# Performance work log

Measured on AMD Instinct MI355X. Metric: run time of the kernel, lower is better.

## Reference

```python
import jax, jax.numpy as jnp
import numpy as np

N = 100000   # nodes
E = 1600000  # edges
D_IN = 256
H = 64       # hidden_dim


def _segment_softmax(e, dst, n):
    # e: [E, heads]; softmax over edges sharing the same dst node
    m = jax.ops.segment_max(e, dst, num_segments=n)
    m = jnp.where(jnp.isfinite(m), m, jnp.zeros_like(m))
    ex = jnp.exp(e - m[dst])
    s = jax.ops.segment_sum(ex, dst, num_segments=n)
    return ex / (s[dst] + 1e-16)


def gat_conv(x, edge_index, W, att_src, att_dst, bias, heads, odim):
    # PyG GATConv, concat=False (mean over heads), with self-loops, neg_slope=0.2
    n = x.shape[0]
    loop = jnp.arange(n, dtype=edge_index.dtype)
    src = jnp.concatenate([edge_index[0], loop])
    dst = jnp.concatenate([edge_index[1], loop])
    h = (x @ W).reshape(n, heads, odim)                      # [N, heads, odim]
    a_s = jnp.einsum('nhd,hd->nh', h, att_src)               # [N, heads]
    a_d = jnp.einsum('nhd,hd->nh', h, att_dst)
    e = jax.nn.leaky_relu(a_s[src] + a_d[dst], 0.2)          # [E+N, heads]
    alpha = _segment_softmax(e, dst, n)
    msg = h[src] * alpha[:, :, None]                         # gather + weight
    out = jax.ops.segment_sum(msg, dst, num_segments=n)      # scatter-reduce
    return out.mean(axis=1) + bias                           # concat=False -> mean


def gcn_conv(x, edge_index, W, bias):
    # PyG GCNConv with self-loops and symmetric normalization
    n = x.shape[0]
    loop = jnp.arange(n, dtype=edge_index.dtype)
    src = jnp.concatenate([edge_index[0], loop])
    dst = jnp.concatenate([edge_index[1], loop])
    deg = jax.ops.segment_sum(jnp.ones(src.shape[0], x.dtype), dst, num_segments=n)
    dinv = jnp.where(deg > 0, deg ** -0.5, jnp.zeros_like(deg))
    norm = dinv[src] * dinv[dst]                             # [E+N]
    h = x @ W
    return jax.ops.segment_sum(h[src] * norm[:, None], dst, num_segments=n) + bias


def setup_inputs() -> dict:
    key = jax.random.key(0)
    ks = jax.random.split(key, 16)
    f = lambda k, shp, s=0.05: (jax.random.normal(k, shp, dtype=jnp.float32) * s)
    inp = {
        'x': jax.random.normal(ks[0], (N, D_IN), dtype=jnp.float32),
        'edge_index': jax.random.randint(ks[1], (2, E), 0, N, dtype=jnp.int64),
        # GAT layer 1: heads=4, out=H
        'W1': f(ks[2], (D_IN, 4 * H)), 'a1s': f(ks[3], (4, H)), 'a1d': f(ks[4], (4, H)),
        'b1': jnp.zeros((H,), jnp.float32),
        # GAT layer 2: heads=2, out=H
        'W2': f(ks[5], (H, 2 * H)), 'a2s': f(ks[6], (2, H)), 'a2d': f(ks[7], (2, H)),
        'b2': jnp.zeros((H,), jnp.float32),
        # GCN layer: H -> H//2
        'Wg': f(ks[8], (H, H // 2)), 'bg': jnp.zeros((H // 2,), jnp.float32),
        # MLP head: H//2 -> H//4 -> 1
        'Wh1': f(ks[9], (H // 2, H // 4)), 'bh1': jnp.zeros((H // 4,), jnp.float32),
        'Wh2': f(ks[10], (H // 4, 1)), 'bh2': jnp.zeros((1,), jnp.float32),
    }
    return inp


def reference(x, edge_index, W1, a1s, a1d, b1, W2, a2s, a2d, b2, Wg, bg, Wh1, bh1, Wh2, bh2):
    h1 = jax.nn.relu(gat_conv(x, edge_index, W1, a1s, a1d, b1, heads=4, odim=H))
    h2 = jax.nn.relu(gat_conv(h1, edge_index, W2, a2s, a2d, b2, heads=2, odim=H))
    h3 = jax.nn.relu(gcn_conv(h2, edge_index, Wg, bg))
    z = jax.nn.relu(h3 @ Wh1 + bh1)
    svi = jax.nn.sigmoid(z @ Wh2 + bh2)
    return svi.squeeze(-1)
```

## Files before the change

### kernel.cpp

```cpp
#include <hip/hip_runtime.h>
#include <math.h>

static inline int cdiv(int a, int b){ return (a + b - 1) / b; }

typedef __attribute__((ext_vector_type(8))) short short8_t;
typedef __attribute__((ext_vector_type(4))) float f32x4;
typedef __attribute__((ext_vector_type(2))) float f32x2;

static __device__ inline unsigned short f2bf(float f) {
    union { float f; unsigned u; } v; v.f = f;
    unsigned r = v.u + 0x7fff + ((v.u >> 16) & 1);
    return (unsigned short)(r >> 16);
}

static __device__ inline unsigned char f2fp8(float f) {
    union { float f; unsigned u; } v; v.f = f;
    unsigned s = (v.u >> 24) & 0x80u;
    v.u &= 0x7fffffffu;
    v.f = fminf(v.f, 448.f);
    unsigned out;
    if (v.u >= (121u << 23)) {
        unsigned u = v.u + 0x7FFFFu + ((v.u >> 20) & 1u);
        out = (((u >> 23) - 120u) << 3) | ((u >> 20) & 7u);
    } else {
        out = (unsigned)(v.f * 512.f + 0.5f);
    }
    return (unsigned char)(out | s);
}

static __device__ inline float fp8_1(unsigned b) {
    unsigned s = (b & 0x80u) << 24;
    unsigned em = b & 0x7fu;
    union { unsigned u; float f; } n;
    n.u = (((em >> 3) + 120u) << 23) | ((em & 7u) << 20);
    float mag = (em >= 8u) ? n.f : (float)em * 0.001953125f;
    union { unsigned u; float f; } r; r.f = mag; r.u |= s;
    return r.f;
}

static __device__ __forceinline__ f32x2 fp8lo(unsigned v) {
#if __has_builtin(__builtin_amdgcn_cvt_pk_f32_fp8)
    return __builtin_amdgcn_cvt_pk_f32_fp8((int)v, false);
#else
    f32x2 r; r[0] = fp8_1(v & 0xff); r[1] = fp8_1((v >> 8) & 0xff); return r;
#endif
}
static __device__ __forceinline__ f32x2 fp8hi(unsigned v) {
#if __has_builtin(__builtin_amdgcn_cvt_pk_f32_fp8)
    return __builtin_amdgcn_cvt_pk_f32_fp8((int)v, true);
#else
    f32x2 r; r[0] = fp8_1((v >> 16) & 0xff); r[1] = fp8_1(v >> 24); return r;
#endif
}


__global__ __launch_bounds__(256) void k_count_deg_win(const int* __restrict__ dst, int E,
        int* __restrict__ deg, int wsize) {
    int win   = blockIdx.x & 7;
    int chunk = blockIdx.x >> 3;
    int lo = win * wsize, hi = lo + wsize;
    int base = (chunk * 256 + threadIdx.x) * 4;
    if (base + 3 < E) {
        int4 d = *(const int4*)(dst + base);
        if (d.x >= lo && d.x < hi) atomicAdd(&deg[d.x], 1);
        if (d.y >= lo && d.y < hi) atomicAdd(&deg[d.y], 1);
        if (d.z >= lo && d.z < hi) atomicAdd(&deg[d.z], 1);
        if (d.w >= lo && d.w < hi) atomicAdd(&deg[d.w], 1);
    } else {
        for (int k = 0; k < 4; k++) {
            int e = base + k;
            if (e < E) { int d = dst[e]; if (d >= lo && d < hi) atomicAdd(&deg[d], 1); }
        }
    }
}

__global__ void k_scan_partial(const int* __restrict__ deg, int n, int* __restrict__ partial) {
    __shared__ int sd[256];
    int base = blockIdx.x * 1024;
    int sum = 0;
    for (int i = threadIdx.x; i < 1024; i += 256) {
        int idx = base + i;
        if (idx < n) sum += deg[idx] + 1;
    }
    sd[threadIdx.x] = sum;
    __syncthreads();
    for (int s = 128; s > 0; s >>= 1) {
        if (threadIdx.x < s) sd[threadIdx.x] += sd[threadIdx.x + s];
        __syncthreads();
    }
    if (threadIdx.x == 0) partial[blockIdx.x] = sd[0];
}

__global__ void k_scan_top(int* __restrict__ partial, int nb, int* __restrict__ offs, int n) {
    if (blockIdx.x == 0 && threadIdx.x == 0) {
        int run = 0;
        for (int i = 0; i < nb; i++) { int v = partial[i]; partial[i] = run; run += v; }
        offs[n] = run;
    }
}

__global__ void k_scan_final(const int* __restrict__ deg, int n,
                             const int* __restrict__ partial, int* __restrict__ offs,
                             int* __restrict__ cursor, int* __restrict__ csr,
                             float* __restrict__ dinv) {
    __shared__ int sd[256];
    int tid = threadIdx.x;
    int base = blockIdx.x * 1024;
    int v[4]; int s0 = 0;
    #pragma unroll
    for (int j = 0; j < 4; j++) {
        int idx = base + tid*4 + j;
        v[j] = (idx < n) ? (deg[idx] + 1) : 0;
        s0 += v[j];
    }
    sd[tid] = s0;
    __syncthreads();
    for (int st = 1; st < 256; st <<= 1) {
        int t = (tid >= st) ? sd[tid - st] : 0;
        __syncthreads();
        sd[tid] += t;
        __syncthreads();
    }
    int ex = (tid > 0 ? sd[tid - 1] : 0) + partial[blockIdx.x];
    #pragma unroll
    for (int j = 0; j < 4; j++) {
        int idx = base + tid*4 + j;
        if (idx < n) {
            offs[idx]   = ex;
            cursor[idx] = ex;
            dinv[idx]   = rsqrtf((float)v[j]);
            csr[ex + v[j] - 1] = idx;
        }
        ex += v[j];
    }
}

__global__ __launch_bounds__(256) void k_fill_csr_win(const int* __restrict__ src,
        const int* __restrict__ dst, int E,
        int* __restrict__ cursor, int* __restrict__ csr, int wsize) {
    int win   = blockIdx.x & 7;
    int chunk = blockIdx.x >> 3;
    int lo = win * wsize, hi = lo + wsize;
    int base = (chunk * 256 + threadIdx.x) * 4;
    if (base + 3 < E) {
        int4 d = *(const int4*)(dst + base);
        bool ix = d.x >= lo && d.x < hi, iy = d.y >= lo && d.y < hi;
        bool iz = d.z >= lo && d.z < hi, iw = d.w >= lo && d.w < hi;
        if (ix | iy | iz | iw) {
            int4 s = *(const int4*)(src + base);
            if (ix) { int p = atomicAdd(&cursor[d.x], 1); csr[p] = s.x; }
            if (iy) { int p = atomicAdd(&cursor[d.y], 1); csr[p] = s.y; }
            if (iz) { int p = atomicAdd(&cursor[d.z], 1); csr[p] = s.z; }
            if (iw) { int p = atomicAdd(&cursor[d.w], 1); csr[p] = s.w; }
        }
    } else {
        for (int k = 0; k < 4; k++) {
            int e = base + k;
            if (e < E) {
                int d = dst[e];
                if (d >= lo && d < hi) { int p = atomicAdd(&cursor[d], 1); csr[p] = src[e]; }
            }
        }
    }
}


__global__ void k_prep_all(const float* __restrict__ W1, const float* __restrict__ W2,
                           const float* __restrict__ Wg, unsigned short* __restrict__ W1t,
                           unsigned short* __restrict__ W2t, unsigned short* __restrict__ Wgt) {
    int t = blockIdx.x * 256 + threadIdx.x;
    if (t < 65536) {
        int k = t >> 8, c = t & 255;
        W1t[c * 256 + k] = f2bf(W1[t]);
    }
    if (t < 8192) {
        int k = t >> 7, c = t & 127;
        W2t[c * 64 + k] = f2bf(W2[t]);
    }
    if (t < 2048) {
        int k = t >> 5, c = t & 31;
        Wgt[c * 64 + k] = f2bf(Wg[t]);
    }
}

__global__ __launch_bounds__(512) void k_gemm1_mfma(const float* __restrict__ A,
        const unsigned short* __restrict__ Bt, const float* __restrict__ att_s_g,
        const float* __restrict__ att_d_g, unsigned char* __restrict__ C,
        float* __restrict__ out_as, float* __restrict__ out_ad, int M) {
    constexpr int LDP = 40;
    __shared__ __align__(16) unsigned short As[128 * LDP];
    __shared__ __align__(16) unsigned short Bs[256 * LDP];
    __shared__ float att_l[512];
    int tid = threadIdx.x;
    int bm = blockIdx.x * 128;
    int wave = tid >> 6, lane = tid & 63;
    int wr = wave >> 1, wc = wave & 1;
    int lg = lane >> 4, lr = lane & 15;

    att_l[tid] = (tid < 256) ? att_s_g[tid] : att_d_g[tid - 256];

    f32x4 acc[2][8] = {};

    for (int k0 = 0; k0 < 256; k0 += 32) {
        __syncthreads();
        {
            int row = tid >> 2, part = tid & 3;
            int gr = bm + row;
            float4 v0, v1;
            if (gr < M) {
                const float4* p = (const float4*)(A + (size_t)gr * 256 + k0 + part * 8);
                v0 = p[0]; v1 = p[1];
            } else {
                v0 = make_float4(0.f,0.f,0.f,0.f); v1 = v0;
            }
            unsigned short* w = &As[row * LDP + part * 8];
            w[0]=f2bf(v0.x); w[1]=f2bf(v0.y); w[2]=f2bf(v0.z); w[3]=f2bf(v0.w);
            w[4]=f2bf(v1.x); w[5]=f2bf(v1.y); w[6]=f2bf(v1.z); w[7]=f2bf(v1.w);
        }
        {
            int col = tid >> 1, part = tid & 1;
            const uint4* p = (const uint4*)(Bt + (size_t)col * 256 + k0 + part * 16);
            uint4 u0 = p[0], u1 = p[1];
            *(uint4*)&Bs[col * LDP + part * 16]     = u0;
            *(uint4*)&Bs[col * LDP + part * 16 + 8] = u1;
        }
        __syncthreads();
        short8_t a[2], b[8];
        #pragma unroll
        for (int i = 0; i < 2; i++)
            a[i] = *(const short8_t*)&As[(wr * 32 + i * 16 + lr) * LDP + lg * 8];
        #pragma unroll
        for (int j = 0; j < 8; j++)
            b[j] = *(const short8_t*)&Bs[(wc * 128 + j * 16 + lr) * LDP + lg * 8];
        #pragma unroll
        for (int i = 0; i < 2; i++)
            #pragma unroll
            for (int j = 0; j < 8; j++)
                acc[i][j] = __builtin_amdgcn_mfma_f32_16x16x32_bf16(a[i], b[j], acc[i][j], 0, 0, 0);
    }
    float ws[8], wd[8];
    #pragma unroll
    for (int j = 0; j < 8; j++) {
        int c = wc * 128 + j * 16 + lr;
        ws[j] = att_l[c]; wd[j] = att_l[256 + c];
    }
    #pragma unroll
    for (int i = 0; i < 2; i++) {
        #pragma unroll
        for (int b2 = 0; b2 < 4; b2++) {
            int row = bm + wr * 32 + i * 16 + lg * 4 + b2;
            #pragma unroll
            for (int j = 0; j < 8; j++) {
                int col = wc * 128 + j * 16 + lr;
                if (row < M) C[(size_t)row * 256 + col] = f2fp8(acc[i][j][b2]);
            }
            float s0=0.f, s1=0.f, d0=0.f, d1=0.f;
            #pragma unroll
            for (int j = 0; j < 4; j++) { float v = acc[i][j][b2];   s0 += v*ws[j];   d0 += v*wd[j]; }
            #pragma unroll
            for (int j = 4; j < 8; j++) { float v = acc[i][j][b2];   s1 += v*ws[j];   d1 += v*wd[j]; }
            #pragma unroll
            for (int off = 1; off < 16; off <<= 1) {
                s0 += __shfl_xor(s0, off); s1 += __shfl_xor(s1, off);
                d0 += __shfl_xor(d0, off); d1 += __shfl_xor(d1, off);
            }
            if (lr == 0 && row < M) {
                out_as[row * 4 + wc * 2]     = s0;
                out_as[row * 4 + wc * 2 + 1] = s1;
                out_ad[row * 4 + wc * 2]     = d0;
                out_ad[row * 4 + wc * 2 + 1] = d1;
            }
        }
    }
}


template<int NC, bool ATT>
__global__ __launch_bounds__(256) void k_gemm_k64_mfma(const float* __restrict__ A,
        const unsigned short* __restrict__ Bt,
        const float* __restrict__ att_s_g, const float* __restrict__ att_d_g,
        unsigned char* __restrict__ C, float* __restrict__ out_as,
        float* __restrict__ out_ad, int M) {
    constexpr int NF  = NC / 16;
    constexpr int LDP = 72;
    __shared__ __align__(16) unsigned short As[64 * LDP];
    __shared__ __align__(16) unsigned short Bs[NC * LDP];
    __shared__ float att_l[ATT ? 2 * NC : 1];
    int tid = threadIdx.x;
    int bm = blockIdx.x * 64;
    int wave = tid >> 6, lane = tid & 63, lg = lane >> 4, lr = lane & 15;

    if constexpr (ATT) {
        if (tid < 2 * NC)
            att_l[tid] = (tid < NC) ? att_s_g[tid] : att_d_g[tid - NC];
    }
    {
        int row = tid >> 2, part = tid & 3;
        int gr = bm + row;
        float4 v0, v1, v2, v3;
        if (gr < M) {
            const float4* p = (const float4*)(A + (size_t)gr * 64 + part * 16);
            v0 = p[0]; v1 = p[1]; v2 = p[2]; v3 = p[3];
        } else {
            v0 = make_float4(0.f,0.f,0.f,0.f); v1 = v0; v2 = v0; v3 = v0;
        }
        unsigned short* w = &As[row * LDP + part * 16];
        w[0]=f2bf(v0.x);  w[1]=f2bf(v0.y);  w[2]=f2bf(v0.z);  w[3]=f2bf(v0.w);
        w[4]=f2bf(v1.x);  w[5]=f2bf(v1.y);  w[6]=f2bf(v1.z);  w[7]=f2bf(v1.w);
        w[8]=f2bf(v2.x);  w[9]=f2bf(v2.y);  w[10]=f2bf(v2.z); w[11]=f2bf(v2.w);
        w[12]=f2bf(v3.x); w[13]=f2bf(v3.y); w[14]=f2bf(v3.z); w[15]=f2bf(v3.w);
    }
    for (int i = tid; i < NC * 8; i += 256) {
        int c = i >> 3, part = i & 7;
        *(uint4*)&Bs[c * LDP + part * 8] = *(const uint4*)(Bt + (size_t)c * 64 + part * 8);
    }
    __syncthreads();

    f32x4 acc[NF] = {};
    short8_t a0 = *(const short8_t*)&As[(wave * 16 + lr) * LDP + lg * 8];
    short8_t a1 = *(const short8_t*)&As[(wave * 16 + lr) * LDP + 32 + lg * 8];
    #pragma unroll
    for (int j = 0; j < NF; j++) {
        short8_t b0 = *(const short8_t*)&Bs[(j * 16 + lr) * LDP + lg * 8];
        short8_t b1 = *(const short8_t*)&Bs[(j * 16 + lr) * LDP + 32 + lg * 8];
        acc[j] = __builtin_amdgcn_mfma_f32_16x16x32_bf16(a0, b0, acc[j], 0, 0, 0);
        acc[j] = __builtin_amdgcn_mfma_f32_16x16x32_bf16(a1, b1, acc[j], 0, 0, 0);
    }
    float ws[NF], wd[NF];
    if constexpr (ATT) {
        #pragma unroll
        for (int j = 0; j < NF; j++) { ws[j] = att_l[j * 16 + lr]; wd[j] = att_l[NC + j * 16 + lr]; }
    }
    #pragma unroll
    for (int b2 = 0; b2 < 4; b2++) {
        int row = bm + wave * 16 + lg * 4 + b2;
        #pragma unroll
        for (int j = 0; j < NF; j++)
            if (row < M) C[(size_t)row * NC + j * 16 + lr] = f2fp8(acc[j][b2]);
        if constexpr (ATT) {
            float s0=0.f, s1=0.f, d0=0.f, d1=0.f;
            #pragma unroll
            for (int j = 0; j < 4; j++) { float v = acc[j][b2]; s0 += v*ws[j]; d0 += v*wd[j]; }
            #pragma unroll
            for (int j = 4; j < 8; j++) { float v = acc[j][b2]; s1 += v*ws[j]; d1 += v*wd[j]; }
            #pragma unroll
            for (int off = 1; off < 16; off <<= 1) {
                s0 += __shfl_xor(s0, off); s1 += __shfl_xor(s1, off);
                d0 += __shfl_xor(d0, off); d1 += __shfl_xor(d1, off);
            }
            if (lr == 0 && row < M) {
                out_as[row * 2]     = s0;
                out_as[row * 2 + 1] = s1;
                out_ad[row * 2]     = d0;
                out_ad[row * 2 + 1] = d1;
            }
        }
    }
}


template<int HEADS>
__global__ __launch_bounds__(256) void k_gat_fused(const unsigned char* __restrict__ hpre,
        const float* __restrict__ as_n, const float* __restrict__ ad_n,
        const float* __restrict__ bias,
        const int* __restrict__ offs, const int* __restrict__ csr,
        float* __restrict__ out, int n_nodes) {
    __shared__ int   s_off[4][64];
    __shared__ float s_p[4][64 * HEADS];
    int wif  = threadIdx.x >> 6;
    int lane = threadIdx.x & 63;
    int n = blockIdx.x * 4 + wif;
    if (n >= n_nodes) return;
    const int beg = offs[n];
    const int deg = offs[n + 1] - beg;

    int h_id, dq;
    if constexpr (HEADS == 4) { h_id = lane >> 4; dq = lane & 15; }
    else                      { h_id = lane >> 5; dq = lane & 31; }
    const int lane_off = h_id * 64 + dq * 4;

    float adv[HEADS];
    if constexpr (HEADS == 4) {
        float4 t = *(const float4*)(ad_n + (size_t)n * 4);
        adv[0]=t.x; adv[1]=t.y; adv[2]=t.z; adv[3]=t.w;
    } else {
        float2 t = *(const float2*)(ad_n + (size_t)n * 2);
        adv[0]=t.x; adv[1]=t.y;
    }

    float sumh = 0.f;
    float acc[HEADS] = {};

    for (int j0 = 0; j0 < deg; j0 += 64) {
        int j = j0 + lane;
        int cnt = min(64, deg - j0);
        if (j < deg) {
            int s = csr[beg + j];
            s_off[wif][lane] = s * (HEADS * 64);
            float ev[HEADS];
            if constexpr (HEADS == 4) {
                float4 t = *(const float4*)(as_n + (size_t)s * 4);
                ev[0]=t.x; ev[1]=t.y; ev[2]=t.z; ev[3]=t.w;
            } else {
                float2 t = *(const float2*)(as_n + (size_t)s * 2);
                ev[0]=t.x; ev[1]=t.y;
            }
            #pragma unroll
            for (int h = 0; h < HEADS; h++) {
                float e = ev[h] + adv[h];
                e = fmaxf(e, 0.2f * e);
                s_p[wif][lane * HEADS + h] = __expf(e);
            }
        }
        #pragma unroll 4
        for (int q = 0; q < cnt; q++) {
            int off = s_off[wif][q];
            float p = s_p[wif][q * HEADS + h_id];
            sumh += p;
            if constexpr (HEADS == 4) {
                unsigned v = *(const unsigned*)(hpre + off + lane_off);
                f32x2 l = fp8lo(v), h2 = fp8hi(v);
                acc[0] += p * l[0]; acc[1] += p * l[1];
                acc[2] += p * h2[0]; acc[3] += p * h2[1];
            } else {
                unsigned v = *(const unsigned short*)(hpre + off + (lane_off >> 1));
                f32x2 l = fp8lo(v);
                acc[0] += p * l[0]; acc[1] += p * l[1];
            }
        }
    }
    float inv = 1.0f / (sumh + 1e-16f);
    float r[HEADS];
    #pragma unroll
    for (int c = 0; c < HEADS; c++) r[c] = acc[c] * inv;
    if constexpr (HEADS == 4) {
        #pragma unroll
        for (int c = 0; c < 4; c++) {
            r[c] += __shfl_xor(r[c], 16);
            r[c] += __shfl_xor(r[c], 32);
            r[c] *= 0.25f;
        }
        if (h_id == 0) {
            float4 b = *(const float4*)(bias + dq * 4);
            float4 o;
            o.x = fmaxf(r[0] + b.x, 0.f); o.y = fmaxf(r[1] + b.y, 0.f);
            o.z = fmaxf(r[2] + b.z, 0.f); o.w = fmaxf(r[3] + b.w, 0.f);
            *(float4*)(out + (size_t)n * 64 + dq * 4) = o;
        }
    } else {
        #pragma unroll
        for (int c = 0; c < 2; c++) {
            r[c] += __shfl_xor(r[c], 32);
            r[c] *= 0.5f;
        }
        if (h_id == 0) {
            float2 b = *(const float2*)(bias + dq * 2);
            float2 o;
            o.x = fmaxf(r[0] + b.x, 0.f); o.y = fmaxf(r[1] + b.y, 0.f);
            *(float2*)(out + (size_t)n * 64 + dq * 2) = o;
        }
    }
}


__global__ __launch_bounds__(256) void k_gcn_agg(const unsigned char* __restrict__ hpre,
        const float* __restrict__ dinv, const float* __restrict__ bias,
        const int* __restrict__ offs, const int* __restrict__ csr,
        float* __restrict__ out, int n_nodes) {
    int gid = blockIdx.x * 256 + threadIdx.x;
    int n = gid >> 3, q = gid & 7;
    if (n >= n_nodes) return;
    const int beg = offs[n], end = offs[n + 1];
    float4 acc = make_float4(0.f,0.f,0.f,0.f);
    #pragma unroll 4
    for (int j = beg; j < end; j++) {
        int s = csr[j];
        float ds = dinv[s];
        unsigned v = *(const unsigned*)(hpre + (size_t)s * 32 + q * 4);
        f32x2 l = fp8lo(v), h2 = fp8hi(v);
        acc.x += ds * l[0]; acc.y += ds * l[1];
        acc.z += ds * h2[0]; acc.w += ds * h2[1];
    }
    float dn = dinv[n];
    float4 b = *(const float4*)(bias + q * 4);
    float4 o;
    o.x = fmaxf(acc.x * dn + b.x, 0.f); o.y = fmaxf(acc.y * dn + b.y, 0.f);
    o.z = fmaxf(acc.z * dn + b.z, 0.f); o.w = fmaxf(acc.w * dn + b.w, 0.f);
    *(float4*)(out + (size_t)n * 32 + q * 4) = o;
}


__global__ __launch_bounds__(256) void k_mlp(const float* __restrict__ h3,
        const float* __restrict__ Wh1, const float* __restrict__ bh1,
        const float* __restrict__ Wh2, const float* __restrict__ bh2,
        float* __restrict__ out, int n_nodes) {
    __shared__ float w1[512];
    __shared__ float w2[16];
    __shared__ float b1s[16];
    __shared__ float b2s;
    int tid = threadIdx.x;
    for (int i = tid; i < 512; i += 256) w1[i] = Wh1[i];
    if (tid < 16) { w2[tid] = Wh2[tid]; b1s[tid] = bh1[tid]; }
    if (tid == 0) b2s = bh2[0];
    __syncthreads();
    int n = blockIdx.x * 256 + tid;
    if (n >= n_nodes) return;
    float x[32];
    const float4* p = (const float4*)(h3 + (size_t)n * 32);
    #pragma unroll
    for (int q = 0; q < 8; q++) { float4 v = p[q]; x[4*q] = v.x; x[4*q+1] = v.y; x[4*q+2] = v.z; x[4*q+3] = v.w; }
    float acc2 = b2s;
    #pragma unroll
    for (int j = 0; j < 16; j++) {
        float z = b1s[j];
        #pragma unroll
        for (int k = 0; k < 32; k++) z += x[k] * w1[k * 16 + j];
        z = fmaxf(z, 0.f);
        acc2 += z * w2[j];
    }
    out[n] = 1.0f / (1.0f + expf(-acc2));
}


extern "C" void kernel_launch(void* const* d_in, const int* in_sizes, int n_in,
                              void* d_out, int out_size, void* d_ws, size_t ws_size,
                              hipStream_t stream) {
    const float* x   = (const float*)d_in[0];
    const int*   ei  = (const int*)d_in[1];
    const float* W1  = (const float*)d_in[2];
    const float* a1s = (const float*)d_in[3];
    const float* a1d = (const float*)d_in[4];
    const float* b1  = (const float*)d_in[5];
    const float* W2  = (const float*)d_in[6];
    const float* a2s = (const float*)d_in[7];
    const float* a2d = (const float*)d_in[8];
    const float* b2  = (const float*)d_in[9];
    const float* Wg  = (const float*)d_in[10];
    const float* bg  = (const float*)d_in[11];
    const float* Wh1 = (const float*)d_in[12];
    const float* bh1 = (const float*)d_in[13];
    const float* Wh2 = (const float*)d_in[14];
    const float* bh2 = (const float*)d_in[15];

    const int N = in_sizes[0] / 256;
    const int E = in_sizes[1] / 2;
    const int* srcs = ei;
    const int* dsts = ei + E;

    float* R0   = (float*)d_ws;
    float* R1   = R0 + (size_t)N * 256;
    float* R2   = R1 + (size_t)N * 64;
    float* As_  = R2 + (size_t)N * 64;
    float* Ad_  = As_ + (size_t)N * 4;
    float* dinv = Ad_ + (size_t)N * 4;
    int* deg    = (int*)(dinv + N);
    int* offs   = deg + N;
    int* cursor = offs + (N + 1);
    int* csr    = cursor + N;
    int* parts  = csr + (E + N);
    unsigned short* W1t = (unsigned short*)(parts + 256);
    unsigned short* W2t = W1t + 65536;
    unsigned short* Wgt = W2t + 8192;
    unsigned char*  HP  = (unsigned char*)R0;

    int wsize = cdiv(N, 8);
    hipMemsetAsync(deg, 0, (size_t)N * sizeof(int), stream);
    k_count_deg_win<<<cdiv(E, 1024) * 8, 256, 0, stream>>>(dsts, E, deg, wsize);
    int nch = cdiv(N, 1024);
    k_scan_partial<<<nch, 256, 0, stream>>>(deg, N, parts);
    k_scan_top<<<1, 64, 0, stream>>>(parts, nch, offs, N);
    k_scan_final<<<nch, 256, 0, stream>>>(deg, N, parts, offs, cursor, csr, dinv);
    k_fill_csr_win<<<cdiv(E, 1024) * 8, 256, 0, stream>>>(srcs, dsts, E, cursor, csr, wsize);

    k_prep_all<<<256, 256, 0, stream>>>(W1, W2, Wg, W1t, W2t, Wgt);

    k_gemm1_mfma<<<cdiv(N, 128), 512, 0, stream>>>(x, W1t, a1s, a1d, HP, As_, Ad_, N);
    k_gat_fused<4><<<cdiv(N, 4), 256, 0, stream>>>(HP, As_, Ad_, b1, offs, csr, R1, N);

    k_gemm_k64_mfma<128, true><<<cdiv(N, 64), 256, 0, stream>>>(R1, W2t, a2s, a2d, HP, As_, Ad_, N);
    k_gat_fused<2><<<cdiv(N, 4), 256, 0, stream>>>(HP, As_, Ad_, b2, offs, csr, R2, N);

    k_gemm_k64_mfma<32, false><<<cdiv(N, 64), 256, 0, stream>>>(R2, Wgt, nullptr, nullptr, HP, nullptr, nullptr, N);
    k_gcn_agg<<<cdiv(N * 8, 256), 256, 0, stream>>>(HP, dinv, bg, offs, csr, R1, N);

    k_mlp<<<cdiv(N, 256), 256, 0, stream>>>(R1, Wh1, bh1, Wh2, bh2, (float*)d_out, N);
}
```

Baseline: 404.7 us.

## Fuse prep/scan launches, pack two nodes per wave in GAT2, fuse GCN with MLP

Folds the weight-transpose prep into the degree-count kernel and removes the single-thread scan_top kernel by having each scan_final block reduce its prefix from the partials. Layer-2 GAT now processes two nodes per wave, so all 64 lanes do useful work with 4-byte fp8 loads instead of 2-byte ones. The GCN aggregation is fused with the MLP head using cross-lane shuffles, which removes a kernel launch and the h3 round trip through memory. The costs are redundant prefix summation in every scan block and more shuffle work in the fused GCN kernel.

```diff
diff --git a/kernel.cpp b/kernel.cpp
--- a/kernel.cpp
+++ b/kernel.cpp
@@ -54,8 +54,18 @@
 }
 
 
-__global__ __launch_bounds__(256) void k_count_deg_win(const int* __restrict__ dst, int E,
-        int* __restrict__ deg, int wsize) {
+__global__ __launch_bounds__(256) void k_count_prep(const int* __restrict__ dst, int E,
+        int* __restrict__ deg, int wsize, int fillBlocks,
+        const float* __restrict__ W1, const float* __restrict__ W2,
+        const float* __restrict__ Wg, unsigned short* __restrict__ W1t,
+        unsigned short* __restrict__ W2t, unsigned short* __restrict__ Wgt) {
+    if (blockIdx.x >= fillBlocks) {
+        int t = (blockIdx.x - fillBlocks) * 256 + threadIdx.x;
+        if (t < 65536) { int k = t >> 8, c = t & 255; W1t[c * 256 + k] = f2bf(W1[t]); }
+        if (t < 8192)  { int k = t >> 7, c = t & 127; W2t[c * 64 + k]  = f2bf(W2[t]); }
+        if (t < 2048)  { int k = t >> 5, c = t & 31;  Wgt[c * 64 + k]  = f2bf(Wg[t]); }
+        return;
+    }
     int win   = blockIdx.x & 7;
     int chunk = blockIdx.x >> 3;
     int lo = win * wsize, hi = lo + wsize;
@@ -91,20 +101,22 @@
     if (threadIdx.x == 0) partial[blockIdx.x] = sd[0];
 }
 
-__global__ void k_scan_top(int* __restrict__ partial, int nb, int* __restrict__ offs, int n) {
-    if (blockIdx.x == 0 && threadIdx.x == 0) {
-        int run = 0;
-        for (int i = 0; i < nb; i++) { int v = partial[i]; partial[i] = run; run += v; }
-        offs[n] = run;
-    }
-}
-
 __global__ void k_scan_final(const int* __restrict__ deg, int n,
                              const int* __restrict__ partial, int* __restrict__ offs,
                              int* __restrict__ cursor, int* __restrict__ csr,
                              float* __restrict__ dinv) {
     __shared__ int sd[256];
     int tid = threadIdx.x;
+    int pre = 0;
+    for (int i = tid; i < (int)blockIdx.x; i += 256) pre += partial[i];
+    sd[tid] = pre;
+    __syncthreads();
+    for (int s = 128; s > 0; s >>= 1) {
+        if (tid < s) sd[tid] += sd[tid + s];
+        __syncthreads();
+    }
+    int base_pre = sd[0];
+    __syncthreads();
     int base = blockIdx.x * 1024;
     int v[4]; int s0 = 0;
     #pragma unroll
@@ -121,7 +133,7 @@
         sd[tid] += t;
         __syncthreads();
     }
-    int ex = (tid > 0 ? sd[tid - 1] : 0) + partial[blockIdx.x];
+    int ex = (tid > 0 ? sd[tid - 1] : 0) + base_pre;
     #pragma unroll
     for (int j = 0; j < 4; j++) {
         int idx = base + tid*4 + j;
@@ -133,6 +145,7 @@
         }
         ex += v[j];
     }
+    if (blockIdx.x == gridDim.x - 1 && tid == 255) offs[n] = ex;
 }
 
 __global__ __launch_bounds__(256) void k_fill_csr_win(const int* __restrict__ src,
@@ -164,25 +177,6 @@
     }
 }
 
-
-__global__ void k_prep_all(const float* __restrict__ W1, const float* __restrict__ W2,
-                           const float* __restrict__ Wg, unsigned short* __restrict__ W1t,
-                           unsigned short* __restrict__ W2t, unsigned short* __restrict__ Wgt) {
-    int t = blockIdx.x * 256 + threadIdx.x;
-    if (t < 65536) {
-        int k = t >> 8, c = t & 255;
-        W1t[c * 256 + k] = f2bf(W1[t]);
-    }
-    if (t < 8192) {
-        int k = t >> 7, c = t & 127;
-        W2t[c * 64 + k] = f2bf(W2[t]);
-    }
-    if (t < 2048) {
-        int k = t >> 5, c = t & 31;
-        Wgt[c * 64 + k] = f2bf(Wg[t]);
-    }
-}
-
 __global__ __launch_bounds__(512) void k_gemm1_mfma(const float* __restrict__ A,
         const unsigned short* __restrict__ Bt, const float* __restrict__ att_s_g,
         const float* __restrict__ att_d_g, unsigned char* __restrict__ C,
@@ -359,14 +353,13 @@
 }
 
 
-template<int HEADS>
-__global__ __launch_bounds__(256) void k_gat_fused(const unsigned char* __restrict__ hpre,
+__global__ __launch_bounds__(256) void k_gat_fused4(const unsigned char* __restrict__ hpre,
         const float* __restrict__ as_n, const float* __restrict__ ad_n,
         const float* __restrict__ bias,
         const int* __restrict__ offs, const int* __restrict__ csr,
         float* __restrict__ out, int n_nodes) {
     __shared__ int   s_off[4][64];
-    __shared__ float s_p[4][64 * HEADS];
+    __shared__ float s_p[4][64 * 4];
     int wif  = threadIdx.x >> 6;
     int lane = threadIdx.x & 63;
     int n = blockIdx.x * 4 + wif;
@@ -374,100 +367,147 @@
     const int beg = offs[n];
     const int deg = offs[n + 1] - beg;
 
-    int h_id, dq;
-    if constexpr (HEADS == 4) { h_id = lane >> 4; dq = lane & 15; }
-    else                      { h_id = lane >> 5; dq = lane & 31; }
+    int h_id = lane >> 4, dq = lane & 15;
     const int lane_off = h_id * 64 + dq * 4;
 
-    float adv[HEADS];
-    if constexpr (HEADS == 4) {
-        float4 t = *(const float4*)(ad_n + (size_t)n * 4);
-        adv[0]=t.x; adv[1]=t.y; adv[2]=t.z; adv[3]=t.w;
-    } else {
-        float2 t = *(const float2*)(ad_n + (size_t)n * 2);
-        adv[0]=t.x; adv[1]=t.y;
-    }
+    float4 t = *(const float4*)(ad_n + (size_t)n * 4);
+    float adv[4] = {t.x, t.y, t.z, t.w};
 
     float sumh = 0.f;
-    float acc[HEADS] = {};
+    float acc[4] = {};
 
     for (int j0 = 0; j0 < deg; j0 += 64) {
         int j = j0 + lane;
         int cnt = min(64, deg - j0);
         if (j < deg) {
             int s = csr[beg + j];
-            s_off[wif][lane] = s * (HEADS * 64);
-            float ev[HEADS];
-            if constexpr (HEADS == 4) {
-                float4 t = *(const float4*)(as_n + (size_t)s * 4);
-                ev[0]=t.x; ev[1]=t.y; ev[2]=t.z; ev[3]=t.w;
-            } else {
-                float2 t = *(const float2*)(as_n + (size_t)s * 2);
-                ev[0]=t.x; ev[1]=t.y;
-            }
-            #pragma unroll
-            for (int h = 0; h < HEADS; h++) {
+            s_off[wif][lane] = s * 256;
+            float4 tv = *(const float4*)(as_n + (size_t)s * 4);
+            float ev[4] = {tv.x, tv.y, tv.z, tv.w};
+            #pragma unroll
+            for (int h = 0; h < 4; h++) {
                 float e = ev[h] + adv[h];
                 e = fmaxf(e, 0.2f * e);
-                s_p[wif][lane * HEADS + h] = __expf(e);
+                s_p[wif][lane * 4 + h] = __expf(e);
             }
         }
         #pragma unroll 4
         for (int q = 0; q < cnt; q++) {
             int off = s_off[wif][q];
-            float p = s_p[wif][q * HEADS + h_id];
+            float p = s_p[wif][q * 4 + h_id];
             sumh += p;
-            if constexpr (HEADS == 4) {
-                unsigned v = *(const unsigned*)(hpre + off + lane_off);
-                f32x2 l = fp8lo(v), h2 = fp8hi(v);
-                acc[0] += p * l[0]; acc[1] += p * l[1];
-                acc[2] += p * h2[0]; acc[3] += p * h2[1];
-            } else {
-                unsigned v = *(const unsigned short*)(hpre + off + (lane_off >> 1));
-                f32x2 l = fp8lo(v);
-                acc[0] += p * l[0]; acc[1] += p * l[1];
-            }
+            unsigned v = *(const unsigned*)(hpre + off + lane_off);
+            f32x2 l = fp8lo(v), h2 = fp8hi(v);
+            acc[0] += p * l[0]; acc[1] += p * l[1];
+            acc[2] += p * h2[0]; acc[3] += p * h2[1];
         }
     }
     float inv = 1.0f / (sumh + 1e-16f);
-    float r[HEADS];
-    #pragma unroll
-    for (int c = 0; c < HEADS; c++) r[c] = acc[c] * inv;
-    if constexpr (HEADS == 4) {
-        #pragma unroll
-        for (int c = 0; c < 4; c++) {
-            r[c] += __shfl_xor(r[c], 16);
-            r[c] += __shfl_xor(r[c], 32);
-            r[c] *= 0.25f;
-        }
-        if (h_id == 0) {
-            float4 b = *(const float4*)(bias + dq * 4);
-            float4 o;
-            o.x = fmaxf(r[0] + b.x, 0.f); o.y = fmaxf(r[1] + b.y, 0.f);
-            o.z = fmaxf(r[2] + b.z, 0.f); o.w = fmaxf(r[3] + b.w, 0.f);
-            *(float4*)(out + (size_t)n * 64 + dq * 4) = o;
-        }
-    } else {
-        #pragma unroll
-        for (int c = 0; c < 2; c++) {
-            r[c] += __shfl_xor(r[c], 32);
-            r[c] *= 0.5f;
-        }
-        if (h_id == 0) {
-            float2 b = *(const float2*)(bias + dq * 2);
-            float2 o;
-            o.x = fmaxf(r[0] + b.x, 0.f); o.y = fmaxf(r[1] + b.y, 0.f);
-            *(float2*)(out + (size_t)n * 64 + dq * 2) = o;
-        }
-    }
-}
-
-
-__global__ __launch_bounds__(256) void k_gcn_agg(const unsigned char* __restrict__ hpre,
+    float r[4];
+    #pragma unroll
+    for (int c = 0; c < 4; c++) r[c] = acc[c] * inv;
+    #pragma unroll
+    for (int c = 0; c < 4; c++) {
+        r[c] += __shfl_xor(r[c], 16);
+        r[c] += __shfl_xor(r[c], 32);
+        r[c] *= 0.25f;
+    }
+    if (h_id == 0) {
+        float4 b = *(const float4*)(bias + dq * 4);
+        float4 o;
+        o.x = fmaxf(r[0] + b.x, 0.f); o.y = fmaxf(r[1] + b.y, 0.f);
+        o.z = fmaxf(r[2] + b.z, 0.f); o.w = fmaxf(r[3] + b.w, 0.f);
+        *(float4*)(out + (size_t)n * 64 + dq * 4) = o;
+    }
+}
+
+
+__global__ __launch_bounds__(256) void k_gat_fused2(const unsigned char* __restrict__ hpre,
+        const float* __restrict__ as_n, const float* __restrict__ ad_n,
+        const float* __restrict__ bias,
+        const int* __restrict__ offs, const int* __restrict__ csr,
+        float* __restrict__ out, int n_nodes) {
+    __shared__ int   s_off[4][2][32];
+    __shared__ float s_p[4][2][64];
+    int wif  = threadIdx.x >> 6;
+    int lane = threadIdx.x & 63;
+    int half = lane >> 5;
+    int l    = lane & 31;
+    int n = blockIdx.x * 8 + wif * 2 + half;
+    bool act = n < n_nodes;
+    int beg = 0, deg = 0;
+    float adv0 = 0.f, adv1 = 0.f;
+    if (act) {
+        beg = offs[n];
+        deg = offs[n + 1] - beg;
+        float2 t = *(const float2*)(ad_n + (size_t)n * 2);
+        adv0 = t.x; adv1 = t.y;
+    }
+    int h_id = l >> 4, dq = l & 15;
+    const int lane_off = h_id * 64 + dq * 4;
+
+    float sumh = 0.f;
+    float acc[4] = {};
+
+    for (int j0 = 0; j0 < deg; j0 += 32) {
+        int j = j0 + l;
+        int cnt = min(32, deg - j0);
+        if (j < deg) {
+            int s = csr[beg + j];
+            s_off[wif][half][l] = s * 128;
+            float2 t = *(const float2*)(as_n + (size_t)s * 2);
+            float e0 = t.x + adv0; e0 = fmaxf(e0, 0.2f * e0);
+            float e1 = t.y + adv1; e1 = fmaxf(e1, 0.2f * e1);
+            s_p[wif][half][l * 2]     = __expf(e0);
+            s_p[wif][half][l * 2 + 1] = __expf(e1);
+        }
+        #pragma unroll 4
+        for (int q = 0; q < cnt; q++) {
+            int off = s_off[wif][half][q];
+            float p = s_p[wif][half][q * 2 + h_id];
+            sumh += p;
+            unsigned v = *(const unsigned*)(hpre + off + lane_off);
+            f32x2 lo = fp8lo(v), hi = fp8hi(v);
+            acc[0] += p * lo[0]; acc[1] += p * lo[1];
+            acc[2] += p * hi[0]; acc[3] += p * hi[1];
+        }
+    }
+    float inv = 1.0f / (sumh + 1e-16f);
+    float r[4];
+    #pragma unroll
+    for (int c = 0; c < 4; c++) r[c] = acc[c] * inv;
+    #pragma unroll
+    for (int c = 0; c < 4; c++) {
+        r[c] += __shfl_xor(r[c], 16);
+        r[c] *= 0.5f;
+    }
+    if (act && h_id == 0) {
+        float4 b = *(const float4*)(bias + dq * 4);
+        float4 o;
+        o.x = fmaxf(r[0] + b.x, 0.f); o.y = fmaxf(r[1] + b.y, 0.f);
+        o.z = fmaxf(r[2] + b.z, 0.f); o.w = fmaxf(r[3] + b.w, 0.f);
+        *(float4*)(out + (size_t)n * 64 + dq * 4) = o;
+    }
+}
+
+
+__global__ __launch_bounds__(256) void k_gcn_mlp(const unsigned char* __restrict__ hpre,
         const float* __restrict__ dinv, const float* __restrict__ bias,
         const int* __restrict__ offs, const int* __restrict__ csr,
+        const float* __restrict__ Wh1, const float* __restrict__ bh1,
+        const float* __restrict__ Wh2, const float* __restrict__ bh2,
         float* __restrict__ out, int n_nodes) {
-    int gid = blockIdx.x * 256 + threadIdx.x;
+    __shared__ float w1[512];
+    __shared__ float w2[16];
+    __shared__ float b1s[16];
+    __shared__ float b2s;
+    int tid = threadIdx.x;
+    for (int i = tid; i < 512; i += 256) w1[i] = Wh1[i];
+    if (tid < 16) { w2[tid] = Wh2[tid]; b1s[tid] = bh1[tid]; }
+    if (tid == 0) b2s = bh2[0];
+    __syncthreads();
+
+    int gid = blockIdx.x * 256 + tid;
     int n = gid >> 3, q = gid & 7;
     if (n >= n_nodes) return;
     const int beg = offs[n], end = offs[n + 1];
@@ -483,42 +523,25 @@
     }
     float dn = dinv[n];
     float4 b = *(const float4*)(bias + q * 4);
-    float4 o;
-    o.x = fmaxf(acc.x * dn + b.x, 0.f); o.y = fmaxf(acc.y * dn + b.y, 0.f);
-    o.z = fmaxf(acc.z * dn + b.z, 0.f); o.w = fmaxf(acc.w * dn + b.w, 0.f);
-    *(float4*)(out + (size_t)n * 32 + q * 4) = o;
-}
-
-
-__global__ __launch_bounds__(256) void k_mlp(const float* __restrict__ h3,
-        const float* __restrict__ Wh1, const float* __restrict__ bh1,
-        const float* __restrict__ Wh2, const float* __restrict__ bh2,
-        float* __restrict__ out, int n_nodes) {
-    __shared__ float w1[512];
-    __shared__ float w2[16];
-    __shared__ float b1s[16];
-    __shared__ float b2s;
-    int tid = threadIdx.x;
-    for (int i = tid; i < 512; i += 256) w1[i] = Wh1[i];
-    if (tid < 16) { w2[tid] = Wh2[tid]; b1s[tid] = bh1[tid]; }
-    if (tid == 0) b2s = bh2[0];
-    __syncthreads();
-    int n = blockIdx.x * 256 + tid;
-    if (n >= n_nodes) return;
-    float x[32];
-    const float4* p = (const float4*)(h3 + (size_t)n * 32);
-    #pragma unroll
-    for (int q = 0; q < 8; q++) { float4 v = p[q]; x[4*q] = v.x; x[4*q+1] = v.y; x[4*q+2] = v.z; x[4*q+3] = v.w; }
+    float x0 = fmaxf(acc.x * dn + b.x, 0.f);
+    float x1 = fmaxf(acc.y * dn + b.y, 0.f);
+    float x2 = fmaxf(acc.z * dn + b.z, 0.f);
+    float x3 = fmaxf(acc.w * dn + b.w, 0.f);
+
+    float pz[16];
+    const float* w1r = w1 + q * 64;
+    #pragma unroll
+    for (int jj = 0; jj < 16; jj++)
+        pz[jj] = x0 * w1r[jj] + x1 * w1r[16 + jj] + x2 * w1r[32 + jj] + x3 * w1r[48 + jj];
+    #pragma unroll
+    for (int off = 1; off < 8; off <<= 1)
+        #pragma unroll
+        for (int jj = 0; jj < 16; jj++) pz[jj] += __shfl_xor(pz[jj], off);
     float acc2 = b2s;
     #pragma unroll
-    for (int j = 0; j < 16; j++) {
-        float z = b1s[j];
-        #pragma unroll
-        for (int k = 0; k < 32; k++) z += x[k] * w1[k * 16 + j];
-        z = fmaxf(z, 0.f);
-        acc2 += z * w2[j];
-    }
-    out[n] = 1.0f / (1.0f + expf(-acc2));
+    for (int jj = 0; jj < 16; jj++)
+        acc2 += fmaxf(pz[jj] + b1s[jj], 0.f) * w2[jj];
+    if (q == 0) out[n] = 1.0f / (1.0f + expf(-acc2));
 }
 
 
@@ -564,24 +587,22 @@
     unsigned char*  HP  = (unsigned char*)R0;
 
     int wsize = cdiv(N, 8);
+    int fillBlocks = cdiv(E, 1024) * 8;
     hipMemsetAsync(deg, 0, (size_t)N * sizeof(int), stream);
-    k_count_deg_win<<<cdiv(E, 1024) * 8, 256, 0, stream>>>(dsts, E, deg, wsize);
+    k_count_prep<<<fillBlocks + 256, 256, 0, stream>>>(dsts, E, deg, wsize, fillBlocks,
+                                                       W1, W2, Wg, W1t, W2t, Wgt);
     int nch = cdiv(N, 1024);
     k_scan_partial<<<nch, 256, 0, stream>>>(deg, N, parts);
-    k_scan_top<<<1, 64, 0, stream>>>(parts, nch, offs, N);
     k_scan_final<<<nch, 256, 0, stream>>>(deg, N, parts, offs, cursor, csr, dinv);
-    k_fill_csr_win<<<cdiv(E, 1024) * 8, 256, 0, stream>>>(srcs, dsts, E, cursor, csr, wsize);
-
-    k_prep_all<<<256, 256, 0, stream>>>(W1, W2, Wg, W1t, W2t, Wgt);
+    k_fill_csr_win<<<fillBlocks, 256, 0, stream>>>(srcs, dsts, E, cursor, csr, wsize);
 
     k_gemm1_mfma<<<cdiv(N, 128), 512, 0, stream>>>(x, W1t, a1s, a1d, HP, As_, Ad_, N);
-    k_gat_fused<4><<<cdiv(N, 4), 256, 0, stream>>>(HP, As_, Ad_, b1, offs, csr, R1, N);
+    k_gat_fused4<<<cdiv(N, 4), 256, 0, stream>>>(HP, As_, Ad_, b1, offs, csr, R1, N);
 
     k_gemm_k64_mfma<128, true><<<cdiv(N, 64), 256, 0, stream>>>(R1, W2t, a2s, a2d, HP, As_, Ad_, N);
-    k_gat_fused<2><<<cdiv(N, 4), 256, 0, stream>>>(HP, As_, Ad_, b2, offs, csr, R2, N);
+    k_gat_fused2<<<cdiv(N, 8), 256, 0, stream>>>(HP, As_, Ad_, b2, offs, csr, R2, N);
 
     k_gemm_k64_mfma<32, false><<<cdiv(N, 64), 256, 0, stream>>>(R2, Wgt, nullptr, nullptr, HP, nullptr, nullptr, N);
-    k_gcn_agg<<<cdiv(N * 8, 256), 256, 0, stream>>>(HP, dinv, bg, offs, csr, R1, N);
-
-    k_mlp<<<cdiv(N, 256), 256, 0, stream>>>(R1, Wh1, bh1, Wh2, bh2, (float*)d_out, N);
-}
+    k_gcn_mlp<<<cdiv(N * 8, 256), 256, 0, stream>>>(HP, dinv, bg, offs, csr,
+                                                    Wh1, bh1, Wh2, bh2, (float*)d_out, N);
+}
```

Result: faster. 377.6 us (-6.7%).
